# Kernel tuning notes

Hardware: AMD Instinct MI355X
Metric: run time of the kernel (lower is better)

The kernel has to match this reference:

```python
import jax, jax.numpy as jnp
import numpy as np

MARGIN = 0.5
EPS = 1e-6  # torch F.pairwise_distance adds eps to the difference before the norm
B, N, D = 1024, 1024, 64


def setup_inputs() -> dict:
    key = jax.random.key(0)
    ka, kp, kn = jax.random.split(key, 3)
    anchor = jax.random.normal(ka, (B, N, D), dtype=jnp.float32)
    positive = jax.random.normal(kp, (B, N, D), dtype=jnp.float32)
    negative = jax.random.normal(kn, (B, N, D), dtype=jnp.float32)
    return {"anchor": anchor, "positive": positive, "negative": negative}


def reference(anchor, positive, negative):
    # pairwise L2 distances over the feature dim -> [B, N]
    dist_pos = jnp.linalg.norm(anchor - positive + EPS, axis=-1)
    dist_neg = jnp.linalg.norm(anchor - negative + EPS, axis=-1)

    # hard-negative mining, vectorized over the batch:
    # candidates are columns where dist_pos - dist_neg + margin > 0;
    # among candidates pick the column with the LARGEST dist_neg
    diff = dist_pos - dist_neg + MARGIN            # [B, N]
    valid = diff > 0                               # [B, N]
    neg_scores = jnp.where(valid, dist_neg, -jnp.inf)
    sel_col = jnp.argmax(neg_scores, axis=1)       # [B] column index of hard negative

    # faithful to the original: negative is indexed on its FIRST dim with the
    # selected column index (requires B == N), yielding [B, N, D]
    hard_neg = negative[sel_col]
    has_valid = jnp.any(valid, axis=1)             # rows the original would keep

    loss = jnp.mean(jax.nn.relu(MARGIN + dist_pos - dist_neg))
    return loss, hard_neg, has_valid
```

## Files before the change

### kernel.cpp

```cpp
#include <hip/hip_runtime.h>
#include <math.h>

#define BB 1024
#define NN 1024
#define DD 64
#define MARGIN_V 0.5f
#define EPS_V 1e-6f
#define QSPLIT 4
#define QCOLS (NN / QSPLIT)

typedef float f32x4 __attribute__((ext_vector_type(4)));

__global__ __launch_bounds__(256) void k_dist(const float* __restrict__ a,
                                              const float* __restrict__ p,
                                              const float* __restrict__ g,
                                              float* __restrict__ ws_loss,
                                              float* __restrict__ ws_score,
                                              int* __restrict__ ws_idx,
                                              int* __restrict__ ws_valid)
{
    const int blk  = blockIdx.x;
    const int b    = blk >> 2;
    const int q    = blk & 3;
    const int tid  = threadIdx.x;
    const int lane = tid & 63;
    const int wave = tid >> 6;
    const int grp  = lane >> 4;
    const int gl   = lane & 15;
    const int group = wave * 4 + grp;

    const int ncol0 = q * QCOLS + group;
    const unsigned int boff0 =
        ((unsigned int)b * (NN * DD) + (unsigned int)ncol0 * DD + (unsigned int)gl * 4) * 4u;

    float loss_acc   = 0.f;
    float best_score = -INFINITY;
    int   best_idx   = 0x7fffffff;

    #pragma unroll 1
    for (int h = 0; h < 2; ++h) {
        f32x4 va[8], vp[8], vg[8];
        #pragma unroll
        for (int i = 0; i < 8; ++i) {
            const unsigned int off = boff0 + (unsigned int)(h * 8 + i) * (16u * DD * 4u);
            asm volatile("global_load_dwordx4 %0, %1, %2"
                         : "=v"(va[i]) : "v"(off), "s"(a) : "memory");
            asm volatile("global_load_dwordx4 %0, %1, %2"
                         : "=v"(vp[i]) : "v"(off), "s"(p) : "memory");
            asm volatile("global_load_dwordx4 %0, %1, %2"
                         : "=v"(vg[i]) : "v"(off), "s"(g) : "memory");
        }
        asm volatile("s_waitcnt vmcnt(0)" ::: "memory");
        __builtin_amdgcn_sched_barrier(0);

        float accp[8], accn[8];
        #pragma unroll
        for (int i = 0; i < 8; ++i) {
            float sp = 0.f, sn = 0.f, t;
            #pragma unroll
            for (int e = 0; e < 4; ++e) {
                t = va[i][e] - vp[i][e] + EPS_V; sp += t * t;
                t = va[i][e] - vg[i][e] + EPS_V; sn += t * t;
            }
            accp[i] = sp; accn[i] = sn;
        }

        #pragma unroll
        for (int i = 0; i < 8; ++i) {
            #pragma unroll
            for (int m = 1; m < 16; m <<= 1) {
                accp[i] += __shfl_xor(accp[i], m, 64);
                accn[i] += __shfl_xor(accn[i], m, 64);
            }
        }

        #pragma unroll
        for (int i = 0; i < 8; ++i) {
            if (gl == i) {
                const int n = ncol0 + (h * 8 + i) * 16;
                const float diff = MARGIN_V + sqrtf(accp[i]) - sqrtf(accn[i]);
                loss_acc += fmaxf(diff, 0.f);
                const float sc = (diff > 0.f) ? sqrtf(accn[i]) : -INFINITY;
                if (sc > best_score || (sc == best_score && n < best_idx)) {
                    best_score = sc; best_idx = n;
                }
            }
        }
    }

    for (int m = 1; m < 64; m <<= 1) {
        loss_acc += __shfl_xor(loss_acc, m, 64);
        const float so = __shfl_xor(best_score, m, 64);
        const int   io = __shfl_xor(best_idx, m, 64);
        if (so > best_score || (so == best_score && io < best_idx)) {
            best_score = so; best_idx = io;
        }
    }

    __shared__ float s_loss[4];
    __shared__ float s_score[4];
    __shared__ int   s_idx[4];
    if ((tid & 63) == 0) {
        s_loss[wave]  = loss_acc;
        s_score[wave] = best_score;
        s_idx[wave]   = best_idx;
    }
    __syncthreads();
    if (tid == 0) {
        float ls = 0.f, bs = -INFINITY;
        int   bi = 0x7fffffff;
        for (int k = 0; k < 4; ++k) {
            ls += s_loss[k];
            const float sc = s_score[k]; const int ix = s_idx[k];
            if (sc > bs || (sc == bs && ix < bi)) { bs = sc; bi = ix; }
        }
        ws_loss[blk]  = ls;
        ws_score[blk] = bs;
        ws_idx[blk]   = bi;
        ws_valid[blk] = (bs > -INFINITY) ? 1 : 0;
    }
}

__global__ __launch_bounds__(1024) void k_merge(const float* __restrict__ ws_loss,
                                                const float* __restrict__ ws_score,
                                                const int* __restrict__ ws_idx,
                                                const int* __restrict__ ws_valid,
                                                float* __restrict__ out_loss,
                                                int* __restrict__ ws_sel,
                                                float* __restrict__ out_hasvalid)
{
    const int b = threadIdx.x;
    float ls = 0.f;
    float bs = -INFINITY;
    int   bi = 0x7fffffff;
    int   av = 0;
    for (int qq = 0; qq < QSPLIT; ++qq) {
        const int idx = b * QSPLIT + qq;
        const float sc = ws_score[idx];
        const int   ix = ws_idx[idx];
        if (sc > bs || (sc == bs && ix < bi)) { bs = sc; bi = ix; }
        ls += ws_loss[idx];
        av |= ws_valid[idx];
    }
    ws_sel[b] = bi;
    out_hasvalid[b] = av ? 1.0f : 0.0f;

    __shared__ float s[16];
    float v = ls;
    for (int m = 1; m < 64; m <<= 1) v += __shfl_xor(v, m, 64);
    if ((b & 63) == 0) s[b >> 6] = v;
    __syncthreads();
    if (b == 0) {
        float tot = 0.f;
        for (int k = 0; k < 16; ++k) tot += s[k];
        out_loss[0] = tot / (float)((size_t)BB * NN);
    }
}

__global__ __launch_bounds__(256) void k_gather(const float* __restrict__ g,
                                                const int* __restrict__ ws_sel,
                                                float* __restrict__ out_hn)
{
    const int b   = blockIdx.y;
    const int sel = ws_sel[b];
    const float* __restrict__ src = g      + (size_t)sel * (NN * DD);
    float* __restrict__       dst = out_hn + (size_t)b   * (NN * DD);
    const int t = blockIdx.x * blockDim.x + threadIdx.x;
    #pragma unroll
    for (int k = 0; k < (NN * DD) / 8192; ++k) {
        const int idx = t + k * 8192;
        __builtin_nontemporal_store(src[idx], dst + idx);
    }
}

extern "C" void kernel_launch(void* const* d_in, const int* in_sizes, int n_in,
                              void* d_out, int out_size, void* d_ws, size_t ws_size,
                              hipStream_t stream) {
    const float* anchor   = (const float*)d_in[0];
    const float* positive = (const float*)d_in[1];
    const float* negative = (const float*)d_in[2];
    float* out = (float*)d_out;

    float* out_loss     = out;
    float* out_hard_neg = out + 1;
    float* out_hasvalid = out + 1 + (size_t)BB * NN * DD;

    float* ws_loss  = (float*)d_ws;
    float* ws_score = ws_loss + BB * QSPLIT;
    int*   ws_idx   = (int*)(ws_score + BB * QSPLIT);
    int*   ws_valid = ws_idx + BB * QSPLIT;
    int*   ws_sel   = ws_valid + BB * QSPLIT;

    k_dist<<<dim3(BB * QSPLIT), dim3(256), 0, stream>>>(anchor, positive, negative,
                                                        ws_loss, ws_score, ws_idx, ws_valid);
    k_merge<<<dim3(1), dim3(1024), 0, stream>>>(ws_loss, ws_score, ws_idx, ws_valid,
                                                out_loss, ws_sel, out_hasvalid);
    k_gather<<<dim3(32, BB), dim3(256), 0, stream>>>(negative, ws_sel, out_hard_neg);
}
```

Baseline: 236.0 us.

## Double-buffer global loads in k_dist with partial vmcnt waits

Replaces the two-phase load-all-then-compute loop in the distance kernel with four phases of 12 loads each. Two register sets alternate, and s_waitcnt vmcnt(12) lets one phase be consumed while the next phase's loads are in flight. The aim is to hide memory latency behind the reduction and shuffle work instead of draining the load queue twice. Register use stays roughly the same (24 vectors live). Correctness now depends on the hand-written asm ordering and the vmcnt counts being exact.

```diff
diff --git a/kernel.cpp b/kernel.cpp
--- a/kernel.cpp
+++ b/kernel.cpp
@@ -10,6 +10,71 @@
 #define QCOLS (NN / QSPLIT)
 
 typedef float f32x4 __attribute__((ext_vector_type(4)));
+
+#define ISSUE12(A0,A1,A2,A3,P0,P1,P2,P3,G0,G1,G2,G3, PH)                      \
+    do {                                                                       \
+        const unsigned int _o0 = boff0 + (unsigned int)((PH)*4 + 0) * 4096u;   \
+        const unsigned int _o1 = boff0 + (unsigned int)((PH)*4 + 1) * 4096u;   \
+        const unsigned int _o2 = boff0 + (unsigned int)((PH)*4 + 2) * 4096u;   \
+        const unsigned int _o3 = boff0 + (unsigned int)((PH)*4 + 3) * 4096u;   \
+        asm volatile(                                                          \
+            "global_load_dwordx4 %0, %12, %16\n\t"                             \
+            "global_load_dwordx4 %4, %12, %17\n\t"                             \
+            "global_load_dwordx4 %8, %12, %18\n\t"                             \
+            "global_load_dwordx4 %1, %13, %16\n\t"                             \
+            "global_load_dwordx4 %5, %13, %17\n\t"                             \
+            "global_load_dwordx4 %9, %13, %18\n\t"                             \
+            "global_load_dwordx4 %2, %14, %16\n\t"                             \
+            "global_load_dwordx4 %6, %14, %17\n\t"                             \
+            "global_load_dwordx4 %10, %14, %18\n\t"                            \
+            "global_load_dwordx4 %3, %15, %16\n\t"                             \
+            "global_load_dwordx4 %7, %15, %17\n\t"                             \
+            "global_load_dwordx4 %11, %15, %18\n\t"                            \
+            : "=&v"(A0), "=&v"(A1), "=&v"(A2), "=&v"(A3),                      \
+              "=&v"(P0), "=&v"(P1), "=&v"(P2), "=&v"(P3),                      \
+              "=&v"(G0), "=&v"(G1), "=&v"(G2), "=&v"(G3)                       \
+            : "v"(_o0), "v"(_o1), "v"(_o2), "v"(_o3),                          \
+              "s"(a), "s"(p), "s"(g)                                           \
+            : "memory");                                                       \
+    } while (0)
+
+#define CONSUME12(A0,A1,A2,A3,P0,P1,P2,P3,G0,G1,G2,G3, PH)                    \
+    do {                                                                       \
+        const f32x4 _va[4] = {A0, A1, A2, A3};                                 \
+        const f32x4 _vp[4] = {P0, P1, P2, P3};                                 \
+        const f32x4 _vg[4] = {G0, G1, G2, G3};                                 \
+        float _accp[4], _accn[4];                                              \
+        _Pragma("unroll")                                                      \
+        for (int _i = 0; _i < 4; ++_i) {                                       \
+            float _sp = 0.f, _sn = 0.f, _t;                                    \
+            _Pragma("unroll")                                                  \
+            for (int _e = 0; _e < 4; ++_e) {                                   \
+                _t = _va[_i][_e] - _vp[_i][_e] + EPS_V; _sp += _t * _t;        \
+                _t = _va[_i][_e] - _vg[_i][_e] + EPS_V; _sn += _t * _t;        \
+            }                                                                  \
+            _accp[_i] = _sp; _accn[_i] = _sn;                                  \
+        }                                                                      \
+        _Pragma("unroll")                                                      \
+        for (int _i = 0; _i < 4; ++_i) {                                       \
+            _Pragma("unroll")                                                  \
+            for (int _m = 1; _m < 16; _m <<= 1) {                              \
+                _accp[_i] += __shfl_xor(_accp[_i], _m, 64);                    \
+                _accn[_i] += __shfl_xor(_accn[_i], _m, 64);                    \
+            }                                                                  \
+        }                                                                      \
+        _Pragma("unroll")                                                      \
+        for (int _i = 0; _i < 4; ++_i) {                                       \
+            if (gl == (PH) * 4 + _i) {                                         \
+                const int _n = ncol0 + ((PH) * 4 + _i) * 16;                   \
+                const float _diff = MARGIN_V + sqrtf(_accp[_i]) - sqrtf(_accn[_i]); \
+                loss_acc += fmaxf(_diff, 0.f);                                 \
+                const float _sc = (_diff > 0.f) ? sqrtf(_accn[_i]) : -INFINITY;\
+                if (_sc > best_score || (_sc == best_score && _n < best_idx)) {\
+                    best_score = _sc; best_idx = _n;                           \
+                }                                                              \
+            }                                                                  \
+        }                                                                      \
+    } while (0)
 
 __global__ __launch_bounds__(256) void k_dist(const float* __restrict__ a,
                                               const float* __restrict__ p,
@@ -37,56 +102,29 @@
     float best_score = -INFINITY;
     int   best_idx   = 0x7fffffff;
 
-    #pragma unroll 1
-    for (int h = 0; h < 2; ++h) {
-        f32x4 va[8], vp[8], vg[8];
-        #pragma unroll
-        for (int i = 0; i < 8; ++i) {
-            const unsigned int off = boff0 + (unsigned int)(h * 8 + i) * (16u * DD * 4u);
-            asm volatile("global_load_dwordx4 %0, %1, %2"
-                         : "=v"(va[i]) : "v"(off), "s"(a) : "memory");
-            asm volatile("global_load_dwordx4 %0, %1, %2"
-                         : "=v"(vp[i]) : "v"(off), "s"(p) : "memory");
-            asm volatile("global_load_dwordx4 %0, %1, %2"
-                         : "=v"(vg[i]) : "v"(off), "s"(g) : "memory");
-        }
-        asm volatile("s_waitcnt vmcnt(0)" ::: "memory");
-        __builtin_amdgcn_sched_barrier(0);
-
-        float accp[8], accn[8];
-        #pragma unroll
-        for (int i = 0; i < 8; ++i) {
-            float sp = 0.f, sn = 0.f, t;
-            #pragma unroll
-            for (int e = 0; e < 4; ++e) {
-                t = va[i][e] - vp[i][e] + EPS_V; sp += t * t;
-                t = va[i][e] - vg[i][e] + EPS_V; sn += t * t;
-            }
-            accp[i] = sp; accn[i] = sn;
-        }
-
-        #pragma unroll
-        for (int i = 0; i < 8; ++i) {
-            #pragma unroll
-            for (int m = 1; m < 16; m <<= 1) {
-                accp[i] += __shfl_xor(accp[i], m, 64);
-                accn[i] += __shfl_xor(accn[i], m, 64);
-            }
-        }
-
-        #pragma unroll
-        for (int i = 0; i < 8; ++i) {
-            if (gl == i) {
-                const int n = ncol0 + (h * 8 + i) * 16;
-                const float diff = MARGIN_V + sqrtf(accp[i]) - sqrtf(accn[i]);
-                loss_acc += fmaxf(diff, 0.f);
-                const float sc = (diff > 0.f) ? sqrtf(accn[i]) : -INFINITY;
-                if (sc > best_score || (sc == best_score && n < best_idx)) {
-                    best_score = sc; best_idx = n;
-                }
-            }
-        }
-    }
+    f32x4 xa0, xa1, xa2, xa3, xp0, xp1, xp2, xp3, xg0, xg1, xg2, xg3;
+    f32x4 ya0, ya1, ya2, ya3, yp0, yp1, yp2, yp3, yg0, yg1, yg2, yg3;
+
+    ISSUE12(xa0,xa1,xa2,xa3, xp0,xp1,xp2,xp3, xg0,xg1,xg2,xg3, 0);
+
+    ISSUE12(ya0,ya1,ya2,ya3, yp0,yp1,yp2,yp3, yg0,yg1,yg2,yg3, 1);
+    asm volatile("s_waitcnt vmcnt(12)" ::: "memory");
+    __builtin_amdgcn_sched_barrier(0);
+    CONSUME12(xa0,xa1,xa2,xa3, xp0,xp1,xp2,xp3, xg0,xg1,xg2,xg3, 0);
+
+    ISSUE12(xa0,xa1,xa2,xa3, xp0,xp1,xp2,xp3, xg0,xg1,xg2,xg3, 2);
+    asm volatile("s_waitcnt vmcnt(12)" ::: "memory");
+    __builtin_amdgcn_sched_barrier(0);
+    CONSUME12(ya0,ya1,ya2,ya3, yp0,yp1,yp2,yp3, yg0,yg1,yg2,yg3, 1);
+
+    ISSUE12(ya0,ya1,ya2,ya3, yp0,yp1,yp2,yp3, yg0,yg1,yg2,yg3, 3);
+    asm volatile("s_waitcnt vmcnt(12)" ::: "memory");
+    __builtin_amdgcn_sched_barrier(0);
+    CONSUME12(xa0,xa1,xa2,xa3, xp0,xp1,xp2,xp3, xg0,xg1,xg2,xg3, 2);
+
+    asm volatile("s_waitcnt vmcnt(0)" ::: "memory");
+    __builtin_amdgcn_sched_barrier(0);
+    CONSUME12(ya0,ya1,ya2,ya3, yp0,yp1,yp2,yp3, yg0,yg1,yg2,yg3, 3);
 
     for (int m = 1; m < 64; m <<= 1) {
         loss_acc += __shfl_xor(loss_acc, m, 64);
```

Result: no change. 238.1 us (+0.9%).
